# Kernel tuning notes

Hardware: AMD Instinct MI355X
Metric: run time of the kernel (lower is better)

## Reference

```python
import jax, jax.numpy as jnp
import numpy as np

N_TOKENS = 16384
D_IN = 1024
D_HID = 4096
D_OUT = 1024
N_EXPERTS = 8


def setup_inputs() -> dict:
    key = jax.random.key(0)
    ks = jax.random.split(key, 7)
    s_in = 1.0 / np.sqrt(D_IN)
    s_hid = 1.0 / np.sqrt(D_HID)
    return {
        "x": jax.random.normal(ks[0], (N_TOKENS, D_IN), dtype=jnp.float32),
        "Wr": jax.random.uniform(ks[1], (D_IN, N_EXPERTS), jnp.float32, -s_in, s_in),
        "br": jax.random.uniform(ks[2], (N_EXPERTS,), jnp.float32, -s_in, s_in),
        "W1": jax.random.uniform(ks[3], (N_EXPERTS, D_IN, D_HID), jnp.float32, -s_in, s_in),
        "b1": jax.random.uniform(ks[4], (N_EXPERTS, D_HID), jnp.float32, -s_in, s_in),
        "W2": jax.random.uniform(ks[5], (N_EXPERTS, D_HID, D_OUT), jnp.float32, -s_hid, s_hid),
        "b2": jax.random.uniform(ks[6], (N_EXPERTS, D_OUT), jnp.float32, -s_hid, s_hid),
    }


def reference(x, Wr, br, W1, b1, W2, b2):
    # Router: softmax over expert logits, hard top-1 dispatch (argmax).
    # Note: output is NOT scaled by routing probs in the original module.
    logits = x @ Wr + br                      # [N, E]
    expert_idx = jnp.argmax(logits, axis=-1)  # [N] (argmax of softmax == argmax of logits)

    n_experts = W1.shape[0]
    out = jnp.zeros((x.shape[0], W2.shape[-1]), dtype=x.dtype)
    # world_size=1 -> all_to_all is identity; masked per-expert dense FFN + combine.
    # Fixed small loop over experts (structurally distinct weights), vectorized over tokens.
    for e in range(n_experts):
        mask = (expert_idx == e)[:, None]                 # [N, 1]
        xe = jnp.where(mask, x, 0.0)                      # zero out tokens not routed here
        y = jax.nn.relu(xe @ W1[e] + b1[e]) @ W2[e] + b2[e]  # [N, D_OUT]
        out = jnp.where(mask, y, out)
    return out
```

## Files before the change

kernel.cpp:

```cpp
#include <hip/hip_runtime.h>
#include <cstdint>

#define NT   16384
#define DIN  1024
#define DHID 4096
#define DOUT 1024
#define NE   8
#define NMT  136
#define NMT2 72

typedef unsigned short u16;
typedef short bf16x8 __attribute__((ext_vector_type(8)));
typedef float f32x4  __attribute__((ext_vector_type(4)));

__device__ __forceinline__ u16 f2b(float f) {
  union { float f; unsigned u; } a; a.f = f;
  unsigned u = a.u;
  return (u16)((u + 0x7FFFu + ((u >> 16) & 1u)) >> 16);
}

__device__ __forceinline__ void gl_lds16(const u16* g, u16* l) {
  __builtin_amdgcn_global_load_lds(
      (const __attribute__((address_space(1))) void*)g,
      (__attribute__((address_space(3))) void*)l,
      16, 0, 0);
}

__device__ __forceinline__ void barrier_raw() {
  asm volatile("" ::: "memory");
  __builtin_amdgcn_s_barrier();
  asm volatile("" ::: "memory");
}
__device__ __forceinline__ void lgkm0() {
  asm volatile("s_waitcnt lgkmcnt(0)" ::: "memory");
  __builtin_amdgcn_sched_barrier(0);
}
__device__ __forceinline__ void vm6() {
  asm volatile("s_waitcnt vmcnt(6)" ::: "memory");
}

__global__ void router_kernel(const float* __restrict__ x, const float* __restrict__ Wr,
                              const float* __restrict__ br, u16* __restrict__ Xb,
                              int* __restrict__ eidx, int* __restrict__ counts) {
  int t = blockIdx.x * 4 + (threadIdx.x >> 6);
  int lane = threadIdx.x & 63;
  const float4* xr = (const float4*)(x + (size_t)t * DIN);
  ushort4* xbr = (ushort4*)(Xb + (size_t)t * DIN);
  float acc[NE];
#pragma unroll
  for (int e = 0; e < NE; e++) acc[e] = 0.f;
#pragma unroll
  for (int i = 0; i < DIN / 256; i++) {
    int q = lane + i * 64;
    float4 xv = xr[q];
    ushort4 o;
    o.x = f2b(xv.x); o.y = f2b(xv.y); o.z = f2b(xv.z); o.w = f2b(xv.w);
    xbr[q] = o;
    const float* wp = Wr + (size_t)q * 4 * NE;
#pragma unroll
    for (int kk = 0; kk < 4; kk++) {
      float xs = (&xv.x)[kk];
      const float4 w0 = *(const float4*)(wp + kk * NE);
      const float4 w1 = *(const float4*)(wp + kk * NE + 4);
      acc[0] += xs * w0.x; acc[1] += xs * w0.y; acc[2] += xs * w0.z; acc[3] += xs * w0.w;
      acc[4] += xs * w1.x; acc[5] += xs * w1.y; acc[6] += xs * w1.z; acc[7] += xs * w1.w;
    }
  }
#pragma unroll
  for (int off = 32; off > 0; off >>= 1) {
#pragma unroll
    for (int e = 0; e < NE; e++) acc[e] += __shfl_down(acc[e], off, 64);
  }
  if (lane == 0) {
    int best = 0; float bv = acc[0] + br[0];
#pragma unroll
    for (int e = 1; e < NE; e++) {
      float v = acc[e] + br[e];
      if (v > bv) { bv = v; best = e; }
    }
    eidx[t] = best;
    atomicAdd(&counts[best], 1);
  }
}

__global__ void zero_kernel(int* __restrict__ p) {
  if (threadIdx.x < 16) p[threadIdx.x] = 0;
}

__global__ void scan_kernel(const int* __restrict__ counts, int* __restrict__ offsets,
                            int4* __restrict__ tiles, int4* __restrict__ tiles2) {
  if (threadIdx.x == 0) {
    int s = 0, nt = 0, nt2 = 0;
    for (int e = 0; e < NE; e++) {
      int c = counts[e];
      offsets[e] = s;
      for (int m0 = 0; m0 < c; m0 += 128) {
        int v = c - m0; if (v > 128) v = 128;
        tiles[nt++] = make_int4(e, s + m0, v, 0);
      }
      for (int m0 = 0; m0 < c; m0 += 256) {
        int v = c - m0; if (v > 256) v = 256;
        tiles2[nt2++] = make_int4(e, s + m0, v, 0);
      }
      s += c;
    }
    offsets[NE] = s;
    while (nt < NMT) tiles[nt++] = make_int4(0, 0, 0, 0);
    while (nt2 < NMT2) tiles2[nt2++] = make_int4(0, 0, 0, 0);
  }
}

__global__ void scatter_kernel(const int* __restrict__ eidx, const int* __restrict__ offsets,
                               int* __restrict__ cursor, int* __restrict__ perm) {
  int t = blockIdx.x * blockDim.x + threadIdx.x;
  if (t >= NT) return;
  int e = eidx[t];
  int pos = offsets[e] + atomicAdd(&cursor[e], 1);
  perm[pos] = t;
}

__global__ void transpose_cvt_all(const float* __restrict__ W1, const float* __restrict__ W2,
                                  u16* __restrict__ W1t, u16* __restrict__ W2t) {
  __shared__ float tile[64][65];
  int bid = blockIdx.x;
  const float* src; u16* dst; int K, H, k0, h0;
  if (bid < NE * 16 * 64) {
    int e = bid >> 10, rem = bid & 1023;
    K = DIN; H = DHID;
    k0 = (rem & 15) * 64; h0 = (rem >> 4) * 64;
    src = W1 + (size_t)e * DIN * DHID; dst = W1t + (size_t)e * DIN * DHID;
  } else {
    bid -= NE * 16 * 64;
    int e = bid >> 10, rem = bid & 1023;
    K = DHID; H = DOUT;
    k0 = (rem >> 4) * 64; h0 = (rem & 15) * 64;
    src = W2 + (size_t)e * DHID * DOUT; dst = W2t + (size_t)e * DHID * DOUT;
  }
  const int tid = threadIdx.x;
#pragma unroll
  for (int i = 0; i < 4; i++) {
    int idx = tid + i * 256;
    int r = idx >> 4;
    int c = (idx & 15) * 4;
    const float4 v = *(const float4*)(src + (size_t)(k0 + r) * H + h0 + c);
    tile[r][c] = v.x; tile[r][c + 1] = v.y; tile[r][c + 2] = v.z; tile[r][c + 3] = v.w;
  }
  __syncthreads();
#pragma unroll
  for (int i = 0; i < 4; i++) {
    int idx = tid + i * 256;
    int r = idx >> 4;
    int c = (idx & 15) * 4;
    ushort4 o;
    o.x = f2b(tile[c][r]); o.y = f2b(tile[c + 1][r]);
    o.z = f2b(tile[c + 2][r]); o.w = f2b(tile[c + 3][r]);
    *(ushort4*)(dst + (size_t)(h0 + r) * K + k0 + c) = o;
  }
}

__global__ __launch_bounds__(256) void moe_gemm2(
    const u16* __restrict__ A, const u16* __restrict__ Bt,
    const float* __restrict__ bias,
    const int* __restrict__ perm, const int4* __restrict__ tiles,
    float* __restrict__ Fout) {
  const int bid = blockIdx.x;
  const int g = bid & 7;
  const int r_ = bid >> 3;
  const int n = r_ & 7;
  const int j = r_ >> 3;
  const int m = g * 17 + j;
  const int4 ti = tiles[m];
  const int valid = ti.z;
  if (valid == 0) return;
  const int e = ti.x;
  const int base_p = ti.y;
  const int n0 = n * 128;
  const int K = DHID, N = DOUT;

  __shared__ u16 sA[2 * 128 * 32];
  __shared__ u16 sB[2 * 128 * 32];

  const int tid = threadIdx.x;
  const int lane = tid & 63;
  const int wave = tid >> 6;
  const int wm = (wave >> 1) * 64;
  const int wn = (wave & 1) * 64;
  const int quad = lane >> 4;
  const int l15 = lane & 15;
  const bool alive = (wm < valid);

  const int rr = lane >> 2;
  const int cb = (lane & 3) * 8;

  const int rA0 = wave * 16 + rr;
  const int rA1 = rA0 + 64;

  int pa0 = base_p + rA0; if (pa0 > NT - 1) pa0 = NT - 1;
  int pa1 = base_p + rA1; if (pa1 > NT - 1) pa1 = NT - 1;
  const u16* aptr0 = A + (size_t)pa0 * K + cb;
  const u16* aptr1 = A + (size_t)pa1 * K + cb;
  const u16* bptr0 = Bt + ((size_t)e * N + n0 + rA0) * K + cb;
  const u16* bptr1 = Bt + ((size_t)e * N + n0 + rA1) * K + cb;

  u16* dA0 = &sA[wave * 512];
  u16* dA1 = &sA[wave * 512 + 2048];
  u16* dB0 = &sB[wave * 512];
  u16* dB1 = &sB[wave * 512 + 2048];

  f32x4 acc[4][4];
#pragma unroll
  for (int mi = 0; mi < 4; mi++)
#pragma unroll
    for (int ni = 0; ni < 4; ni++)
      acc[mi][ni] = (f32x4){0.f, 0.f, 0.f, 0.f};

  const int kiters = K >> 6;
  for (int kt = 0; kt < kiters; kt++) {
    if (kt) __syncthreads();
    gl_lds16(aptr0,      dA0);
    gl_lds16(aptr1,      dA1);
    gl_lds16(bptr0,      dB0);
    gl_lds16(bptr1,      dB1);
    gl_lds16(aptr0 + 32, dA0 + 4096);
    gl_lds16(aptr1 + 32, dA1 + 4096);
    gl_lds16(bptr0 + 32, dB0 + 4096);
    gl_lds16(bptr1 + 32, dB1 + 4096);
    aptr0 += 64; aptr1 += 64; bptr0 += 64; bptr1 += 64;
    __syncthreads();

    if (alive) {
#pragma unroll
      for (int h = 0; h < 2; h++) {
        bf16x8 af[4], bfr[4];
#pragma unroll
        for (int mi = 0; mi < 4; mi++)
          af[mi] = *(const bf16x8*)&sA[h * 4096 + (wm + mi * 16 + l15) * 32 + quad * 8];
#pragma unroll
        for (int ni = 0; ni < 4; ni++)
          bfr[ni] = *(const bf16x8*)&sB[h * 4096 + (wn + ni * 16 + l15) * 32 + quad * 8];
#pragma unroll
        for (int mi = 0; mi < 4; mi++)
#pragma unroll
          for (int ni = 0; ni < 4; ni++)
            acc[mi][ni] = __builtin_amdgcn_mfma_f32_16x16x32_bf16(af[mi], bfr[ni], acc[mi][ni], 0, 0, 0);
      }
    }
  }
  if (!alive) return;

  float bv[4];
#pragma unroll
  for (int ni = 0; ni < 4; ni++)
    bv[ni] = bias[(size_t)e * N + n0 + wn + ni * 16 + l15];

#pragma unroll
  for (int mi = 0; mi < 4; mi++) {
#pragma unroll
    for (int r = 0; r < 4; r++) {
      const int ml = wm + mi * 16 + quad * 4 + r;
      if (ml >= valid) continue;
      const int token = perm[base_p + ml];
      float* orow = Fout + (size_t)token * N + n0 + wn;
#pragma unroll
      for (int ni = 0; ni < 4; ni++)
        orow[ni * 16 + l15] = acc[mi][ni][r] + bv[ni];
    }
  }
}

#define RXA0 0
#define RXA1 8192
#define RXB0 16384
#define RXB1 24576
#define RYA0 32768
#define RYA1 40960
#define RYB0 49152
#define RYB1 57344

__global__ __launch_bounds__(512, 2) void moe_gemm1_8ph(
    const u16* __restrict__ A, const u16* __restrict__ Bt,
    const float* __restrict__ bias, const int* __restrict__ perm,
    const int4* __restrict__ tiles, u16* __restrict__ Hout) {
  const int bid = blockIdx.x;
  const int g = bid & 7;
  const int r_ = bid >> 3;
  const int n = r_ & 15;
  const int j_ = r_ >> 4;
  const int m = g * 9 + j_;
  const int4 ti = tiles[m];
  const int valid = ti.z;
  if (valid == 0) return;
  const int e = ti.x;
  const int base_p = ti.y;
  const int n0 = n * 256;

  __shared__ u16 lds[65536];

  const int tid = threadIdx.x;
  const int lane = tid & 63;
  const int w = tid >> 6;
  const int wr = w >> 2;
  const int wc = w & 3;
  const int quad = lane >> 4;
  const int l15 = lane & 15;
  const bool aliveLo = (valid > wr * 128);
  const bool aliveHi = (valid > wr * 128 + 64);

  const int srow = tid >> 3;
  const int klog = ((tid & 7) << 3) ^ ((srow & 7) << 3);
  int p0 = base_p + srow;        if (p0 > NT - 1) p0 = NT - 1;
  int p1 = base_p + 64 + srow;   if (p1 > NT - 1) p1 = NT - 1;
  int p2 = base_p + 128 + srow;  if (p2 > NT - 1) p2 = NT - 1;
  int p3 = base_p + 192 + srow;  if (p3 > NT - 1) p3 = NT - 1;
  const u16* pA00 = A + (size_t)perm[p0] * DIN + klog;
  const u16* pA01 = A + (size_t)perm[p1] * DIN + klog;
  const u16* pA10 = A + (size_t)perm[p2] * DIN + klog;
  const u16* pA11 = A + (size_t)perm[p3] * DIN + klog;
  const u16* pB00 = Bt + ((size_t)e * DHID + n0 + srow)       * DIN + klog;
  const u16* pB01 = Bt + ((size_t)e * DHID + n0 + 64 + srow)  * DIN + klog;
  const u16* pB10 = Bt + ((size_t)e * DHID + n0 + 128 + srow) * DIN + klog;
  const u16* pB11 = Bt + ((size_t)e * DHID + n0 + 192 + srow) * DIN + klog;

#define STG(RB, P0, P1, KO) \
  do { gl_lds16((P0) + (KO), &lds[(RB) + w * 512]); \
       gl_lds16((P1) + (KO), &lds[(RB) + 4096 + w * 512]); } while (0)

  STG(RXA0, pA00, pA01, 0);
  STG(RXA1, pA10, pA11, 0);
  STG(RXB0, pB00, pB01, 0);
  STG(RXB1, pB10, pB11, 0);
  STG(RYB0, pB00, pB01, 64);
  STG(RYB1, pB10, pB11, 64);
  STG(RYA0, pA00, pA01, 64);
  vm6();
  barrier_raw();

  const int aX = RXA0 + wr * 8192;
  const int bX = RXB0 + (wc >> 1) * 8192;
  const int aY = RYA0 + wr * 8192;
  const int bY = RYB0 + (wc >> 1) * 8192;
  const int swz = (l15 & 7) << 3;
  const int brow = (wc & 1) * 64 + l15;

  bf16x8 aF[4][2], bF[4][2];
  f32x4 acc[8][4];
#pragma unroll
  for (int i = 0; i < 8; i++)
#pragma unroll
    for (int j2 = 0; j2 < 4; j2++) acc[i][j2] = (f32x4){0.f, 0.f, 0.f, 0.f};

#define RDA(BASE, MH) do { if ((MH) ? aliveHi : aliveLo) { _Pragma("unroll") \
  for (int mi = 0; mi < 4; mi++) { _Pragma("unroll") \
    for (int h = 0; h < 2; h++) \
      aF[mi][h] = *(const bf16x8*)&lds[(BASE) + ((MH) * 64 + mi * 16 + l15) * 64 + \
                                       ((h * 32 + quad * 8) ^ swz)]; } } } while (0)

#define RDB2(BASE, NB) do { if (aliveLo) { _Pragma("unroll") \
  for (int ni = 0; ni < 2; ni++) { _Pragma("unroll") \
    for (int h = 0; h < 2; h++) \
      bF[(NB) + ni][h] = *(const bf16x8*)&lds[(BASE) + (brow + ((NB) + ni) * 16) * 64 + \
                                              ((h * 32 + quad * 8) ^ swz)]; } } } while (0)

#define MM(MH, NB) do { if ((MH) ? aliveHi : aliveLo) { \
  __builtin_amdgcn_s_setprio(1); _Pragma("unroll") \
  for (int mi = 0; mi < 4; mi++) { _Pragma("unroll") \
    for (int ni = 0; ni < 2; ni++) { _Pragma("unroll") \
      for (int h = 0; h < 2; h++) \
        acc[(MH) * 4 + mi][(NB) + ni] = __builtin_amdgcn_mfma_f32_16x16x32_bf16( \
            aF[mi][h], bF[(NB) + ni][h], acc[(MH) * 4 + mi][(NB) + ni], 0, 0, 0); } } \
  __builtin_amdgcn_s_setprio(0); } } while (0)

  const int NITER = DIN / 128;
  for (int j = 0; j < NITER; j++) {
    const int ky1 = (2 * j + 1) * 64;
    int t2 = 2 * j + 2; if (t2 > 15) t2 = 15;
    int t3 = 2 * j + 3; if (t3 > 15) t3 = 15;
    const int kx = t2 * 64, ky2 = t3 * 64;
    RDA(aX, 0); RDB2(bX, 0);
    STG(RYA1, pA10, pA11, ky1);
    barrier_raw(); lgkm0();
    MM(0, 0);
    barrier_raw();
    RDB2(bX, 2);
    STG(RXB0, pB00, pB01, kx);
    barrier_raw(); lgkm0();
    MM(0, 2);
    barrier_raw();
    RDA(aX, 1);
    STG(RXB1, pB10, pB11, kx);
    barrier_raw(); lgkm0();
    MM(1, 2);
    barrier_raw();
    STG(RXA0, pA00, pA01, kx);
    barrier_raw(); lgkm0();
    MM(1, 0);
    vm6();
    barrier_raw();
    RDA(aY, 0); RDB2(bY, 0);
    STG(RXA1, pA10, pA11, kx);
    barrier_raw(); lgkm0();
    MM(0, 0);
    barrier_raw();
    RDB2(bY, 2);
    STG(RYB0, pB00, pB01, ky2);
    barrier_raw(); lgkm0();
    MM(0, 2);
    barrier_raw();
    RDA(aY, 1);
    STG(RYB1, pB10, pB11, ky2);
    barrier_raw(); lgkm0();
    MM(1, 2);
    barrier_raw();
    STG(RYA0, pA00, pA01, ky2);
    barrier_raw(); lgkm0();
    MM(1, 0);
    vm6();
    barrier_raw();
  }

  const int col0 = n0 + wc * 64;
  float bv[4];
#pragma unroll
  for (int ni = 0; ni < 4; ni++)
    bv[ni] = bias[(size_t)e * DHID + col0 + ni * 16 + l15];
#pragma unroll
  for (int mi8 = 0; mi8 < 8; mi8++) {
#pragma unroll
    for (int r = 0; r < 4; r++) {
      const int ml = wr * 128 + mi8 * 16 + quad * 4 + r;
      if (ml >= valid) continue;
      u16* orow = Hout + (size_t)(base_p + ml) * DHID + col0;
#pragma unroll
      for (int ni = 0; ni < 4; ni++) {
        float v = acc[mi8][ni][r] + bv[ni];
        v = v > 0.f ? v : 0.f;
        orow[ni * 16 + l15] = f2b(v);
      }
    }
  }
#undef STG
#undef RDA
#undef RDB2
#undef MM
}

__global__ void sentinel_kernel(float* __restrict__ out, int n) {
  int i = blockIdx.x * blockDim.x + threadIdx.x;
  if (i < n) out[i] = 31337.0f;
}

extern "C" void kernel_launch(void* const* d_in, const int* in_sizes, int n_in,
                              void* d_out, int out_size, void* d_ws, size_t ws_size,
                              hipStream_t stream) {
  const float* x  = (const float*)d_in[0];
  const float* Wr = (const float*)d_in[1];
  const float* br = (const float*)d_in[2];
  const float* W1 = (const float*)d_in[3];
  const float* b1 = (const float*)d_in[4];
  const float* W2 = (const float*)d_in[5];
  const float* b2 = (const float*)d_in[6];
  float* out = (float*)d_out;

  const size_t szXb  = (size_t)NT * DIN * 2;
  const size_t szW1t = (size_t)NE * DIN * DHID * 2;
  const size_t szW2t = (size_t)NE * DHID * DOUT * 2;
  const size_t szHid = (size_t)NT * DHID * 2;
  char* ws = (char*)d_ws;
  u16* Xb   = (u16*)ws;
  u16* W1t  = (u16*)(ws + szXb);
  u16* W2t  = (u16*)(ws + szXb + szW1t);
  u16* Hid  = (u16*)(ws + szXb + szW1t + szW2t);
  int* perm = (int*)(ws + szXb + szW1t + szW2t + szHid);
  int* eidx = perm + NT;
  int* ctrl = eidx + NT;
  int* counts  = ctrl;
  int* cursor  = ctrl + 8;
  int* offsets = ctrl + 16;
  int4* tiles   = (int4*)(ctrl + 32);
  int4* tiles2  = tiles + NMT;
  const size_t NEED = szXb + szW1t + szW2t + szHid + (size_t)NT * 4 * 2 + 4096;

  if (ws_size < NEED) {
    sentinel_kernel<<<(out_size + 255) / 256, 256, 0, stream>>>(out, out_size);
    return;
  }

  zero_kernel<<<1, 64, 0, stream>>>(ctrl);
  transpose_cvt_all<<<NE * 16 * 64 * 2, 256, 0, stream>>>(W1, W2, W1t, W2t);
  router_kernel<<<NT / 4, 256, 0, stream>>>(x, Wr, br, Xb, eidx, counts);
  scan_kernel<<<1, 64, 0, stream>>>(counts, offsets, tiles, tiles2);
  scatter_kernel<<<NT / 256, 256, 0, stream>>>(eidx, offsets, cursor, perm);

  moe_gemm1_8ph<<<16 * NMT2, 512, 0, stream>>>(Xb, W1t, b1, perm, tiles2, Hid);
  moe_gemm2<<<8 * NMT, 256, 0, stream>>>(Hid, W2t, b2, perm, tiles, out);
}
```

Baseline: 991.2 us.

## Double-buffer LDS in down-projection GEMM and reorder LDS stores in up-projection

The second (W2) GEMM kernel now uses two LDS buffers. The next K-tile is prefetched with global_load_lds while MFMAs run on the current tile, with one barrier per iteration instead of two. This aims to hide global-load latency, but it doubles LDS use per block, which may reduce occupancy. In the first GEMM's hand-scheduled loop, the B-half LDS stores are moved after the second MFMA group and the next A read, changing the interleaving of stores and compute.

```diff
diff --git a/kernel.cpp b/kernel.cpp
--- a/kernel.cpp
+++ b/kernel.cpp
@@ -177,8 +177,8 @@
   const int n0 = n * 128;
   const int K = DHID, N = DOUT;
 
-  __shared__ u16 sA[2 * 128 * 32];
-  __shared__ u16 sB[2 * 128 * 32];
+  __shared__ u16 sA[2 * 2 * 128 * 32];
+  __shared__ u16 sB[2 * 2 * 128 * 32];
 
   const int tid = threadIdx.x;
   const int lane = tid & 63;
@@ -202,10 +202,18 @@
   const u16* bptr0 = Bt + ((size_t)e * N + n0 + rA0) * K + cb;
   const u16* bptr1 = Bt + ((size_t)e * N + n0 + rA1) * K + cb;
 
-  u16* dA0 = &sA[wave * 512];
-  u16* dA1 = &sA[wave * 512 + 2048];
-  u16* dB0 = &sB[wave * 512];
-  u16* dB1 = &sB[wave * 512 + 2048];
+#define STAGE2(b) do {                                      \
+    u16* ba = &sA[(b) * 8192 + wave * 512];                 \
+    u16* bb = &sB[(b) * 8192 + wave * 512];                 \
+    gl_lds16(aptr0,      ba);                               \
+    gl_lds16(aptr1,      ba + 2048);                        \
+    gl_lds16(bptr0,      bb);                               \
+    gl_lds16(bptr1,      bb + 2048);                        \
+    gl_lds16(aptr0 + 32, ba + 4096);                        \
+    gl_lds16(aptr1 + 32, ba + 2048 + 4096);                 \
+    gl_lds16(bptr0 + 32, bb + 4096);                        \
+    gl_lds16(bptr1 + 32, bb + 2048 + 4096);                 \
+    aptr0 += 64; aptr1 += 64; bptr0 += 64; bptr1 += 64; } while (0)
 
   f32x4 acc[4][4];
 #pragma unroll
@@ -214,30 +222,25 @@
     for (int ni = 0; ni < 4; ni++)
       acc[mi][ni] = (f32x4){0.f, 0.f, 0.f, 0.f};
 
+  STAGE2(0);
+  __syncthreads();
+
+  int cur = 0;
   const int kiters = K >> 6;
   for (int kt = 0; kt < kiters; kt++) {
-    if (kt) __syncthreads();
-    gl_lds16(aptr0,      dA0);
-    gl_lds16(aptr1,      dA1);
-    gl_lds16(bptr0,      dB0);
-    gl_lds16(bptr1,      dB1);
-    gl_lds16(aptr0 + 32, dA0 + 4096);
-    gl_lds16(aptr1 + 32, dA1 + 4096);
-    gl_lds16(bptr0 + 32, dB0 + 4096);
-    gl_lds16(bptr1 + 32, dB1 + 4096);
-    aptr0 += 64; aptr1 += 64; bptr0 += 64; bptr1 += 64;
-    __syncthreads();
-
+    if (kt + 1 < kiters) STAGE2(cur ^ 1);
     if (alive) {
+      const u16* cA = &sA[cur * 8192];
+      const u16* cB = &sB[cur * 8192];
 #pragma unroll
       for (int h = 0; h < 2; h++) {
         bf16x8 af[4], bfr[4];
 #pragma unroll
         for (int mi = 0; mi < 4; mi++)
-          af[mi] = *(const bf16x8*)&sA[h * 4096 + (wm + mi * 16 + l15) * 32 + quad * 8];
+          af[mi] = *(const bf16x8*)&cA[h * 4096 + (wm + mi * 16 + l15) * 32 + quad * 8];
 #pragma unroll
         for (int ni = 0; ni < 4; ni++)
-          bfr[ni] = *(const bf16x8*)&sB[h * 4096 + (wn + ni * 16 + l15) * 32 + quad * 8];
+          bfr[ni] = *(const bf16x8*)&cB[h * 4096 + (wn + ni * 16 + l15) * 32 + quad * 8];
 #pragma unroll
         for (int mi = 0; mi < 4; mi++)
 #pragma unroll
@@ -245,7 +248,10 @@
             acc[mi][ni] = __builtin_amdgcn_mfma_f32_16x16x32_bf16(af[mi], bfr[ni], acc[mi][ni], 0, 0, 0);
       }
     }
-  }
+    __syncthreads();
+    cur ^= 1;
+  }
+#undef STAGE2
   if (!alive) return;
 
   float bv[4];
@@ -382,11 +388,11 @@
     MM(0, 0);
     barrier_raw();
     RDB2(bX, 2);
+    barrier_raw(); lgkm0();
+    MM(0, 2);
+    barrier_raw();
+    RDA(aX, 1);
     STG(RXB0, pB00, pB01, kx);
-    barrier_raw(); lgkm0();
-    MM(0, 2);
-    barrier_raw();
-    RDA(aX, 1);
     STG(RXB1, pB10, pB11, kx);
     barrier_raw(); lgkm0();
     MM(1, 2);
@@ -402,11 +408,11 @@
     MM(0, 0);
     barrier_raw();
     RDB2(bY, 2);
+    barrier_raw(); lgkm0();
+    MM(0, 2);
+    barrier_raw();
+    RDA(aY, 1);
     STG(RYB0, pB00, pB01, ky2);
-    barrier_raw(); lgkm0();
-    MM(0, 2);
-    barrier_raw();
-    RDA(aY, 1);
     STG(RYB1, pB10, pB11, ky2);
     barrier_raw(); lgkm0();
     MM(1, 2);
```

New measurement: 1.065 ms. 7.4% more time.
